# Optimization experiments

Hardware: AMD Instinct MI355X
Metric: run time of the kernel (lower is better)

The kernel has to match this reference:

```python
import jax, jax.numpy as jnp
import numpy as np

B, N, H = 8, 2048, 1024

def setup_inputs() -> dict:
    key = jax.random.key(0)
    ks = jax.random.split(key, 10)
    s = 1.0 / np.sqrt(2 * H)
    return {
        "sem": jax.random.normal(ks[0], (B, N, H), jnp.float32),
        "temp": jax.random.normal(ks[1], (B, N, H), jnp.float32),
        "Wq": jax.random.normal(ks[2], (2 * H, H), jnp.float32) * s,
        "bq": jnp.zeros((H,), jnp.float32),
        "Wk": jax.random.normal(ks[3], (2 * H, H), jnp.float32) * s,
        "bk": jnp.zeros((H,), jnp.float32),
        "Wv": jax.random.normal(ks[4], (2 * H, H), jnp.float32) * s,
        "bv": jnp.zeros((H,), jnp.float32),
        "Wg": jax.random.normal(ks[5], (2 * H, 1), jnp.float32) * s,
        "bg": jnp.zeros((1,), jnp.float32),
    }

def reference(sem, temp, Wq, bq, Wk, bk, Wv, bv, Wg, bg):
    combined = jnp.concatenate([sem, temp], axis=-1)          # [B,N,2H]
    Q = combined @ Wq + bq                                    # [B,N,H]
    K = combined @ Wk + bk
    V = combined @ Wv + bv
    scale = 1.0 / jnp.sqrt(jnp.asarray(Q.shape[-1], Q.dtype))
    scores = jnp.einsum('bqh,bkh->bqk', Q, K) * scale         # [B,N,N]
    attn = jax.nn.softmax(scores, axis=-1)
    gate = jax.nn.sigmoid(combined @ Wg + bg)                 # [B,N,1]
    attn_weights = attn * gate                                # row-wise gate
    fused = jnp.einsum('bqk,bkh->bqh', attn_weights, V)       # [B,N,H]
    return fused + sem, attn_weights.mean(axis=1)             # [B,N,H], [B,N]
```

## Files before the change

kernel.cpp:

```cpp
#include <hip/hip_runtime.h>
#include <stdint.h>
#include <math.h>

#define NB 8
#define NN 2048
#define HH 1024
#define K2 2048
#define MM 16384

typedef unsigned short u16;
typedef __attribute__((ext_vector_type(8))) short short8v;
typedef __attribute__((ext_vector_type(4))) float floatx4;

__device__ __forceinline__ float bf2f(u16 u) { return __uint_as_float(((unsigned)u) << 16); }
__device__ __forceinline__ u16 f2bf(float f) {
  unsigned u = __float_as_uint(f);
  unsigned r = (u + 0x7fffu + ((u >> 16) & 1u)) >> 16;
  return (u16)r;
}

__device__ __forceinline__ void async16(const void* g, void* lds) {
  __builtin_amdgcn_global_load_lds((const __attribute__((address_space(1))) void*)g,
                                   (__attribute__((address_space(3))) void*)lds,
                                   16, 0, 0);
}

__device__ __forceinline__ int xcd_swz(int bid, int nblk) {
  return (bid & 7) * (nblk >> 3) + (bid >> 3);
}

#define SBAR() __builtin_amdgcn_sched_barrier(0)

__device__ __forceinline__ void gemm128_core(const u16* __restrict__ A, int lda,
                                             const u16* __restrict__ Bt, int ldb,
                                             int rowA0, int rowB0, int K,
                                             u16* sA, u16* sB, floatx4 acc[4][4]) {
  const int t = threadIdx.x;
  const int w = t >> 6, l = t & 63;
  const int wr = w >> 1, wc = w & 1;

#pragma unroll
  for (int mi = 0; mi < 4; mi++)
#pragma unroll
    for (int ni = 0; ni < 4; ni++) { floatx4 z = {0.f,0.f,0.f,0.f}; acc[mi][ni] = z; }

  const int srow = l >> 2;
  const int cs = (((l & 3) ^ ((l >> 3) & 3)) << 3);
  const u16* gA0 = A + (size_t)(rowA0 + w * 32 + srow) * lda + cs;
  const u16* gA1 = A + (size_t)(rowA0 + w * 32 + 16 + srow) * lda + cs;
  const u16* gB0 = Bt + (size_t)(rowB0 + w * 32 + srow) * ldb + cs;
  const u16* gB1 = Bt + (size_t)(rowB0 + w * 32 + 16 + srow) * ldb + cs;
  char* dA = (char*)sA + w * 2048 + l * 16;
  char* dB = (char*)sB + w * 2048 + l * 16;

  const int fr = l & 15;
  const int ch = (((l >> 4) ^ ((fr >> 1) & 3)) << 4);
  const int abase = wr * 4096 + fr * 64 + ch;
  const int bbase = wc * 4096 + fr * 64 + ch;

  const int NT = K >> 5;

#define STG128(bi, kt) { const int ko_ = (kt) << 5; const int bo_ = (bi) << 13; \
    async16(gA0 + ko_, dA + bo_); async16(gA1 + ko_, dA + bo_ + 1024);          \
    async16(gB0 + ko_, dB + bo_); async16(gB1 + ko_, dB + bo_ + 1024); }

  STG128(0, 0);
  for (int tt = 0; tt < NT; ++tt) {
    const int bc = tt & 1;
    if (tt + 1 < NT) {
      STG128(bc ^ 1, tt + 1);
      asm volatile("s_waitcnt vmcnt(4)" ::: "memory");
    } else {
      asm volatile("s_waitcnt vmcnt(0)" ::: "memory");
    }
    __builtin_amdgcn_s_barrier();

    const char* a = (const char*)sA + (bc << 13);
    const char* b = (const char*)sB + (bc << 13);
    short8v af[4], bf[4];
#pragma unroll
    for (int mi = 0; mi < 4; mi++) af[mi] = *(const short8v*)(a + abase + mi * 1024);
#pragma unroll
    for (int ni = 0; ni < 4; ni++) bf[ni] = *(const short8v*)(b + bbase + ni * 1024);
    __builtin_amdgcn_s_setprio(1);
#pragma unroll
    for (int mi = 0; mi < 4; mi++)
#pragma unroll
      for (int ni = 0; ni < 4; ni++)
        acc[mi][ni] = __builtin_amdgcn_mfma_f32_16x16x32_bf16(af[mi], bf[ni], acc[mi][ni], 0, 0, 0);
    __builtin_amdgcn_s_setprio(0);
    SBAR();
    __builtin_amdgcn_s_barrier();
  }
#undef STG128
}

__global__ void __launch_bounds__(256) k_prep_gate(const float* __restrict__ sem,
                                                   const float* __restrict__ temp,
                                                   const float* __restrict__ Wg,
                                                   const float* __restrict__ bg,
                                                   u16* __restrict__ X, float* __restrict__ gate) {
  __shared__ float red[4];
  int row = blockIdx.x;
  int t = threadIdx.x, w = t >> 6, l = t & 63;
  const float* s0 = sem + (size_t)row * 1024 + t * 4;
  const float* t0 = temp + (size_t)row * 1024 + t * 4;
  u16* xr = X + (size_t)row * 2048;
  float4 a = *(const float4*)s0;
  float4 b = *(const float4*)t0;
  ushort4 oa = { f2bf(a.x), f2bf(a.y), f2bf(a.z), f2bf(a.w) };
  ushort4 ob = { f2bf(b.x), f2bf(b.y), f2bf(b.z), f2bf(b.w) };
  *(ushort4*)(xr + t * 4) = oa;
  *(ushort4*)(xr + 1024 + t * 4) = ob;
  float4 wa = *(const float4*)(Wg + t * 4);
  float4 wb = *(const float4*)(Wg + 1024 + t * 4);
  float s = a.x * wa.x + a.y * wa.y + a.z * wa.z + a.w * wa.w
          + b.x * wb.x + b.y * wb.y + b.z * wb.z + b.w * wb.w;
#pragma unroll
  for (int off = 32; off > 0; off >>= 1) s += __shfl_xor(s, off);
  if (l == 0) red[w] = s;
  __syncthreads();
  if (t == 0) {
    float tot = red[0] + red[1] + red[2] + red[3] + bg[0];
    gate[row] = 1.f / (1.f + expf(-tot));
  }
}

__global__ void __launch_bounds__(256) k_transpose_w(const float* __restrict__ W,
                                                     u16* __restrict__ Wt) {
  __shared__ float s[32][33];
  int tile = blockIdx.x;
  int nt = tile & 31, kt = tile >> 5;
  int tx = threadIdx.x & 31, ty = threadIdx.x >> 5;
  int n0 = nt << 5, k0 = kt << 5;
#pragma unroll
  for (int j = 0; j < 32; j += 8)
    s[ty + j][tx] = W[(size_t)(k0 + ty + j) * 1024 + (n0 + tx)];
  __syncthreads();
#pragma unroll
  for (int j = 0; j < 32; j += 8)
    Wt[(size_t)(n0 + ty + j) * 2048 + (k0 + tx)] = f2bf(s[tx][ty + j]);
}

__global__ void __launch_bounds__(256, 3) k_proj_qkv(const u16* __restrict__ X,
                                                     const u16* __restrict__ Wt,
                                                     const float* __restrict__ bq,
                                                     const float* __restrict__ bk,
                                                     const float* __restrict__ bv,
                                                     u16* __restrict__ Qb,
                                                     u16* __restrict__ Kb,
                                                     u16* __restrict__ Vt) {
  __shared__ __align__(16) u16 sA[2 * 4096];
  __shared__ __align__(16) u16 sB[2 * 4096];
  int tile = xcd_swz(blockIdx.x, 3072);
  int bm = tile / 24, bn = tile - bm * 24;
  floatx4 acc[4][4];
  gemm128_core(X, K2, Wt, K2, bm * 128, bn * 128, K2, sA, sB, acc);

  const int t = threadIdx.x, w = t >> 6, l = t & 63;
  const int wr = w >> 1, wc = w & 1;
  const int r0 = bm * 128 + wr * 64 + ((l >> 4) << 2);
  const int c0 = (bn & 7) * 128 + wc * 64 + (l & 15);
  const int which = bn >> 3;
  if (which == 2) {
#pragma unroll
    for (int ni = 0; ni < 4; ni++) {
      int h = c0 + ni * 16;
      float bvv = bv[h];
#pragma unroll
      for (int mi = 0; mi < 4; mi++) {
        int rg = r0 + mi * 16;
        int b = rg >> 11, n = rg & 2047;
        ushort4 o = { f2bf(acc[mi][ni][0] + bvv), f2bf(acc[mi][ni][1] + bvv),
                      f2bf(acc[mi][ni][2] + bvv), f2bf(acc[mi][ni][3] + bvv) };
        *(ushort4*)&Vt[((size_t)b * 1024 + h) * 2048 + n] = o;
      }
    }
  } else {
    u16* Out = (which == 0) ? Qb : Kb;
    const float* bias = (which == 0) ? bq : bk;
#pragma unroll
    for (int ni = 0; ni < 4; ni++) {
      int c1 = c0 + ni * 16;
      float bvv = bias[c1];
#pragma unroll
      for (int mi = 0; mi < 4; mi++)
#pragma unroll
        for (int i = 0; i < 4; i++)
          Out[(size_t)(r0 + mi * 16 + i) * 1024 + c1] = f2bf(acc[mi][ni][i] + bvv);
    }
  }
}

__global__ void __launch_bounds__(256, 3) k_scores(const u16* __restrict__ Q, const u16* __restrict__ Kb,
                                                   u16* __restrict__ E, float* __restrict__ lsum) {
  __shared__ __align__(16) u16 sA[2 * 4096];
  __shared__ __align__(16) u16 sB[2 * 4096];
  int tile = xcd_swz(blockIdx.x, 2048);
  int b = tile >> 8, r = tile & 255, bm = r >> 4, bn = r & 15;
  const u16* A = Q + (size_t)b * NN * HH;
  const u16* Bt = Kb + (size_t)b * NN * HH;
  floatx4 acc[4][4];
  gemm128_core(A, HH, Bt, HH, bm * 128, bn * 128, HH, sA, sB, acc);

  u16* Eb = E + (size_t)b * NN * NN;
  float* lb = lsum + b * NN;
  const int t = threadIdx.x, w = t >> 6, l = t & 63;
  const int wr = w >> 1, wc = w & 1;
  const int q0 = bm * 128 + wr * 64 + ((l >> 4) << 2);
  const int k0c = bn * 128 + wc * 64 + (l & 15);
#pragma unroll
  for (int mi = 0; mi < 4; mi++)
#pragma unroll
    for (int i = 0; i < 4; i++) {
      int q = q0 + mi * 16 + i;
      float rs = 0.f;
#pragma unroll
      for (int ni = 0; ni < 4; ni++) {
        float e = expf(acc[mi][ni][i] * 0.03125f);
        Eb[(size_t)q * NN + k0c + ni * 16] = f2bf(e);
        rs += e;
      }
      rs += __shfl_xor(rs, 1);
      rs += __shfl_xor(rs, 2);
      rs += __shfl_xor(rs, 4);
      rs += __shfl_xor(rs, 8);
      if ((l & 15) == 0) atomicAdd(&lb[q], rs);
    }
}

__global__ void __launch_bounds__(256, 3) k_pv(const u16* __restrict__ E, const u16* __restrict__ Vt,
                                               const float* __restrict__ gate, const float* __restrict__ lsum,
                                               const float* __restrict__ sem, float* __restrict__ out) {
  __shared__ __align__(16) u16 sA[2 * 4096];
  __shared__ __align__(16) u16 sB[2 * 4096];
  int tile = xcd_swz(blockIdx.x, 1024);
  int b = tile >> 7, r = tile & 127, bm = r >> 3, bn = r & 7;
  const u16* A = E + (size_t)b * NN * NN;
  const u16* Bt = Vt + (size_t)b * HH * NN;
  floatx4 acc[4][4];
  gemm128_core(A, NN, Bt, NN, bm * 128, bn * 128, NN, sA, sB, acc);

  const int t = threadIdx.x, w = t >> 6, l = t & 63;
  const int wr = w >> 1, wc = w & 1;
  const int q0 = bm * 128 + wr * 64 + ((l >> 4) << 2);
  const int h0 = bn * 128 + wc * 64 + (l & 15);
#pragma unroll
  for (int mi = 0; mi < 4; mi++)
#pragma unroll
    for (int i = 0; i < 4; i++) {
      int q = q0 + mi * 16 + i;
      size_t gq = (size_t)b * NN + q;
      float wq = gate[gq] / lsum[gq];
#pragma unroll
      for (int ni = 0; ni < 4; ni++) {
        int h = h0 + ni * 16;
        out[gq * HH + h] = acc[mi][ni][i] * wq + sem[gq * HH + h];
      }
    }
}

__global__ void __launch_bounds__(256) k_colmean(const u16* __restrict__ E, const float* __restrict__ gate,
                                                 const float* __restrict__ lsum, float* __restrict__ cm) {
  __shared__ float wsh[256];
  int bid = blockIdx.x;
  int b = bid >> 6, rest = bid & 63;
  int ks = rest >> 3, qc = rest & 7;
  int t = threadIdx.x;
  {
    size_t gq = (size_t)b * NN + qc * 256 + t;
    wsh[t] = gate[gq] / lsum[gq];
  }
  __syncthreads();
  int k = ks * 256 + t;
  const u16* Eb = E + ((size_t)b * NN + (size_t)qc * 256) * NN + k;
  float s = 0.f;
  for (int q = 0; q < 256; q++) s += wsh[q] * bf2f(Eb[(size_t)q * NN]);
  atomicAdd(&cm[b * NN + k], s * (1.f / 2048.f));
}

extern "C" void kernel_launch(void* const* d_in, const int* in_sizes, int n_in,
                              void* d_out, int out_size, void* d_ws, size_t ws_size,
                              hipStream_t stream) {
  const float* sem  = (const float*)d_in[0];
  const float* temp = (const float*)d_in[1];
  const float* Wq   = (const float*)d_in[2];
  const float* bq   = (const float*)d_in[3];
  const float* Wk   = (const float*)d_in[4];
  const float* bk   = (const float*)d_in[5];
  const float* Wv   = (const float*)d_in[6];
  const float* bv   = (const float*)d_in[7];
  const float* Wg   = (const float*)d_in[8];
  const float* bg   = (const float*)d_in[9];
  float* out = (float*)d_out;

  char* ws = (char*)d_ws;
  u16* X      = (u16*)ws;
  u16* E      = X;
  u16* WqkvT  = (u16*)(ws + 67108864);
  u16* Qb     = (u16*)(ws + 79691776);
  u16* Kb     = (u16*)(ws + 113246208);
  u16* Vt     = (u16*)(ws + 146800640);
  float* gate = (float*)(ws + 180355072);
  float* lsum = (float*)(ws + 180420608);

  hipMemsetAsync(lsum, 0, 65536, stream);
  hipMemsetAsync(out + 16777216, 0, 65536, stream);

  k_prep_gate<<<16384, 256, 0, stream>>>(sem, temp, Wg, bg, X, gate);
  k_transpose_w<<<2048, 256, 0, stream>>>(Wq, WqkvT);
  k_transpose_w<<<2048, 256, 0, stream>>>(Wk, WqkvT + (size_t)1024 * 2048);
  k_transpose_w<<<2048, 256, 0, stream>>>(Wv, WqkvT + (size_t)2048 * 2048);
  k_proj_qkv<<<3072, 256, 0, stream>>>(X, WqkvT, bq, bk, bv, Qb, Kb, Vt);
  k_scores<<<2048, 256, 0, stream>>>(Qb, Kb, E, lsum);
  k_pv<<<1024, 256, 0, stream>>>(E, Vt, gate, lsum, sem, out);
  k_colmean<<<512, 256, 0, stream>>>(E, gate, lsum, out + 16777216);
}
```

Baseline: 502.2 us.

## Switch GEMM core to 32x32x16 MFMA with triple-buffered LDS pipeline

Replaces the 16x16x32 bf16 MFMA tiles with 32x32x16 MFMAs, each wave holding a 2x2 grid of 32x32 accumulators. LDS fragment reads are restructured to match, and the epilogues of the QKV, scores and PV kernels are remapped to the new accumulator layout. The staging pipeline goes from double to triple buffering, keeping two K-tiles in flight to hide global load latency. The cost is 50% more LDS per block, which may hurt occupancy at 3 blocks per CU. The swizzle and lane mapping must also stay conflict-free and correct.

Measured after the change: 572.7 us. 14.0% more time.

```diff
diff --git a/kernel.cpp b/kernel.cpp
--- a/kernel.cpp
+++ b/kernel.cpp
@@ -10,7 +10,7 @@
 
 typedef unsigned short u16;
 typedef __attribute__((ext_vector_type(8))) short short8v;
-typedef __attribute__((ext_vector_type(4))) float floatx4;
+typedef __attribute__((ext_vector_type(16))) float floatx16;
 
 __device__ __forceinline__ float bf2f(u16 u) { return __uint_as_float(((unsigned)u) << 16); }
 __device__ __forceinline__ u16 f2bf(float f) {
@@ -31,18 +31,20 @@
 
 #define SBAR() __builtin_amdgcn_sched_barrier(0)
 
+#define MFMA32(a, b, c) __builtin_amdgcn_mfma_f32_32x32x16_bf16(a, b, c, 0, 0, 0)
+
 __device__ __forceinline__ void gemm128_core(const u16* __restrict__ A, int lda,
                                              const u16* __restrict__ Bt, int ldb,
                                              int rowA0, int rowB0, int K,
-                                             u16* sA, u16* sB, floatx4 acc[4][4]) {
+                                             u16* sA, u16* sB, floatx16 acc[2][2]) {
   const int t = threadIdx.x;
   const int w = t >> 6, l = t & 63;
   const int wr = w >> 1, wc = w & 1;
 
 #pragma unroll
-  for (int mi = 0; mi < 4; mi++)
-#pragma unroll
-    for (int ni = 0; ni < 4; ni++) { floatx4 z = {0.f,0.f,0.f,0.f}; acc[mi][ni] = z; }
+  for (int mi = 0; mi < 2; mi++)
+#pragma unroll
+    for (int ni = 0; ni < 2; ni++) acc[mi][ni] = (floatx16)(0.f);
 
   const int srow = l >> 2;
   const int cs = (((l & 3) ^ ((l >> 3) & 3)) << 3);
@@ -53,10 +55,10 @@
   char* dA = (char*)sA + w * 2048 + l * 16;
   char* dB = (char*)sB + w * 2048 + l * 16;
 
-  const int fr = l & 15;
-  const int ch = (((l >> 4) ^ ((fr >> 1) & 3)) << 4);
-  const int abase = wr * 4096 + fr * 64 + ch;
-  const int bbase = wc * 4096 + fr * 64 + ch;
+  const int l31 = l & 31;
+  const int arow = (wr * 64 + l31) * 64;
+  const int brow = (wc * 64 + l31) * 64;
+  const int pc0 = (((l >> 5) ^ ((l >> 1) & 3)) << 4);
 
   const int NT = K >> 5;
 
@@ -65,32 +67,43 @@
     async16(gB0 + ko_, dB + bo_); async16(gB1 + ko_, dB + bo_ + 1024); }
 
   STG128(0, 0);
+  STG128(1, 1);
+  int bc = 0, bs = 2;
   for (int tt = 0; tt < NT; ++tt) {
-    const int bc = tt & 1;
-    if (tt + 1 < NT) {
-      STG128(bc ^ 1, tt + 1);
+    if (tt + 2 < NT) {
+      STG128(bs, tt + 2);
+      asm volatile("s_waitcnt vmcnt(8)" ::: "memory");
+    } else if (tt + 1 < NT) {
       asm volatile("s_waitcnt vmcnt(4)" ::: "memory");
     } else {
       asm volatile("s_waitcnt vmcnt(0)" ::: "memory");
     }
     __builtin_amdgcn_s_barrier();
 
-    const char* a = (const char*)sA + (bc << 13);
-    const char* b = (const char*)sB + (bc << 13);
-    short8v af[4], bf[4];
-#pragma unroll
-    for (int mi = 0; mi < 4; mi++) af[mi] = *(const short8v*)(a + abase + mi * 1024);
-#pragma unroll
-    for (int ni = 0; ni < 4; ni++) bf[ni] = *(const short8v*)(b + bbase + ni * 1024);
+    const char* a = (const char*)sA + bc * 8192;
+    const char* b = (const char*)sB + bc * 8192;
+    short8v a00 = *(const short8v*)(a + arow + pc0);
+    short8v a01 = *(const short8v*)(a + arow + (pc0 ^ 32));
+    short8v a10 = *(const short8v*)(a + arow + 2048 + pc0);
+    short8v a11 = *(const short8v*)(a + arow + 2048 + (pc0 ^ 32));
+    short8v b00 = *(const short8v*)(b + brow + pc0);
+    short8v b01 = *(const short8v*)(b + brow + (pc0 ^ 32));
+    short8v b10 = *(const short8v*)(b + brow + 2048 + pc0);
+    short8v b11 = *(const short8v*)(b + brow + 2048 + (pc0 ^ 32));
     __builtin_amdgcn_s_setprio(1);
-#pragma unroll
-    for (int mi = 0; mi < 4; mi++)
-#pragma unroll
-      for (int ni = 0; ni < 4; ni++)
-        acc[mi][ni] = __builtin_amdgcn_mfma_f32_16x16x32_bf16(af[mi], bf[ni], acc[mi][ni], 0, 0, 0);
+    acc[0][0] = MFMA32(a00, b00, acc[0][0]);
+    acc[0][1] = MFMA32(a00, b10, acc[0][1]);
+    acc[1][0] = MFMA32(a10, b00, acc[1][0]);
+    acc[1][1] = MFMA32(a10, b10, acc[1][1]);
+    acc[0][0] = MFMA32(a01, b01, acc[0][0]);
+    acc[0][1] = MFMA32(a01, b11, acc[0][1]);
+    acc[1][0] = MFMA32(a11, b01, acc[1][0]);
+    acc[1][1] = MFMA32(a11, b11, acc[1][1]);
     __builtin_amdgcn_s_setprio(0);
     SBAR();
     __builtin_amdgcn_s_barrier();
+    bc = (bc == 2) ? 0 : bc + 1;
+    bs = (bs == 2) ? 0 : bs + 1;
   }
 #undef STG128
 }
@@ -150,113 +163,117 @@
                                                      u16* __restrict__ Qb,
                                                      u16* __restrict__ Kb,
                                                      u16* __restrict__ Vt) {
-  __shared__ __align__(16) u16 sA[2 * 4096];
-  __shared__ __align__(16) u16 sB[2 * 4096];
+  __shared__ __align__(16) u16 sA[3 * 4096];
+  __shared__ __align__(16) u16 sB[3 * 4096];
   int tile = xcd_swz(blockIdx.x, 3072);
   int bm = tile / 24, bn = tile - bm * 24;
-  floatx4 acc[4][4];
+  floatx16 acc[2][2];
   gemm128_core(X, K2, Wt, K2, bm * 128, bn * 128, K2, sA, sB, acc);
 
   const int t = threadIdx.x, w = t >> 6, l = t & 63;
   const int wr = w >> 1, wc = w & 1;
-  const int r0 = bm * 128 + wr * 64 + ((l >> 4) << 2);
-  const int c0 = (bn & 7) * 128 + wc * 64 + (l & 15);
+  const int l31 = l & 31, lh = l >> 5;
+  const int r0 = bm * 128 + wr * 64;
+  const int c0b = (bn & 7) * 128 + wc * 64;
   const int which = bn >> 3;
   if (which == 2) {
 #pragma unroll
-    for (int ni = 0; ni < 4; ni++) {
-      int h = c0 + ni * 16;
-      float bvv = bv[h];
-#pragma unroll
-      for (int mi = 0; mi < 4; mi++) {
-        int rg = r0 + mi * 16;
-        int b = rg >> 11, n = rg & 2047;
-        ushort4 o = { f2bf(acc[mi][ni][0] + bvv), f2bf(acc[mi][ni][1] + bvv),
-                      f2bf(acc[mi][ni][2] + bvv), f2bf(acc[mi][ni][3] + bvv) };
-        *(ushort4*)&Vt[((size_t)b * 1024 + h) * 2048 + n] = o;
+    for (int mi = 0; mi < 2; mi++)
+#pragma unroll
+      for (int ni = 0; ni < 2; ni++) {
+        int h = c0b + ni * 32 + l31;
+        float bvv = bv[h];
+#pragma unroll
+        for (int g = 0; g < 4; g++) {
+          int rg = r0 + mi * 32 + 8 * g + 4 * lh;
+          int b = rg >> 11, n = rg & 2047;
+          ushort4 o = { f2bf(acc[mi][ni][4 * g + 0] + bvv), f2bf(acc[mi][ni][4 * g + 1] + bvv),
+                        f2bf(acc[mi][ni][4 * g + 2] + bvv), f2bf(acc[mi][ni][4 * g + 3] + bvv) };
+          *(ushort4*)&Vt[((size_t)b * 1024 + h) * 2048 + n] = o;
+        }
       }
-    }
   } else {
     u16* Out = (which == 0) ? Qb : Kb;
     const float* bias = (which == 0) ? bq : bk;
 #pragma unroll
-    for (int ni = 0; ni < 4; ni++) {
-      int c1 = c0 + ni * 16;
-      float bvv = bias[c1];
-#pragma unroll
-      for (int mi = 0; mi < 4; mi++)
-#pragma unroll
-        for (int i = 0; i < 4; i++)
-          Out[(size_t)(r0 + mi * 16 + i) * 1024 + c1] = f2bf(acc[mi][ni][i] + bvv);
-    }
+    for (int mi = 0; mi < 2; mi++)
+#pragma unroll
+      for (int ni = 0; ni < 2; ni++) {
+        int c1 = c0b + ni * 32 + l31;
+        float bvv = bias[c1];
+#pragma unroll
+        for (int r = 0; r < 16; r++) {
+          int row = r0 + mi * 32 + (r & 3) + 8 * (r >> 2) + 4 * lh;
+          Out[(size_t)row * 1024 + c1] = f2bf(acc[mi][ni][r] + bvv);
+        }
+      }
   }
 }
 
 __global__ void __launch_bounds__(256, 3) k_scores(const u16* __restrict__ Q, const u16* __restrict__ Kb,
                                                    u16* __restrict__ E, float* __restrict__ lsum) {
-  __shared__ __align__(16) u16 sA[2 * 4096];
-  __shared__ __align__(16) u16 sB[2 * 4096];
+  __shared__ __align__(16) u16 sA[3 * 4096];
+  __shared__ __align__(16) u16 sB[3 * 4096];
   int tile = xcd_swz(blockIdx.x, 2048);
   int b = tile >> 8, r = tile & 255, bm = r >> 4, bn = r & 15;
   const u16* A = Q + (size_t)b * NN * HH;
   const u16* Bt = Kb + (size_t)b * NN * HH;
-  floatx4 acc[4][4];
+  floatx16 acc[2][2];
   gemm128_core(A, HH, Bt, HH, bm * 128, bn * 128, HH, sA, sB, acc);
 
   u16* Eb = E + (size_t)b * NN * NN;
   float* lb = lsum + b * NN;
   const int t = threadIdx.x, w = t >> 6, l = t & 63;
   const int wr = w >> 1, wc = w & 1;
-  const int q0 = bm * 128 + wr * 64 + ((l >> 4) << 2);
-  const int k0c = bn * 128 + wc * 64 + (l & 15);
-#pragma unroll
-  for (int mi = 0; mi < 4; mi++)
-#pragma unroll
-    for (int i = 0; i < 4; i++) {
-      int q = q0 + mi * 16 + i;
-      float rs = 0.f;
-#pragma unroll
-      for (int ni = 0; ni < 4; ni++) {
-        float e = expf(acc[mi][ni][i] * 0.03125f);
-        Eb[(size_t)q * NN + k0c + ni * 16] = f2bf(e);
-        rs += e;
-      }
+  const int l31 = l & 31, lh = l >> 5;
+  const int q0 = bm * 128 + wr * 64;
+  const int k0c = bn * 128 + wc * 64;
+#pragma unroll
+  for (int mi = 0; mi < 2; mi++)
+#pragma unroll
+    for (int r = 0; r < 16; r++) {
+      int q = q0 + mi * 32 + (r & 3) + 8 * (r >> 2) + 4 * lh;
+      float e0 = expf(acc[mi][0][r] * 0.03125f);
+      float e1 = expf(acc[mi][1][r] * 0.03125f);
+      Eb[(size_t)q * NN + k0c + l31] = f2bf(e0);
+      Eb[(size_t)q * NN + k0c + 32 + l31] = f2bf(e1);
+      float rs = e0 + e1;
       rs += __shfl_xor(rs, 1);
       rs += __shfl_xor(rs, 2);
       rs += __shfl_xor(rs, 4);
       rs += __shfl_xor(rs, 8);
-      if ((l & 15) == 0) atomicAdd(&lb[q], rs);
+      rs += __shfl_xor(rs, 16);
+      if (l31 == 0) atomicAdd(&lb[q], rs);
     }
 }
 
 __global__ void __launch_bounds__(256, 3) k_pv(const u16* __restrict__ E, const u16* __restrict__ Vt,
                                                const float* __restrict__ gate, const float* __restrict__ lsum,
                                                const float* __restrict__ sem, float* __restrict__ out) {
-  __shared__ __align__(16) u16 sA[2 * 4096];
-  __shared__ __align__(16) u16 sB[2 * 4096];
+  __shared__ __align__(16) u16 sA[3 * 4096];
+  __shared__ __align__(16) u16 sB[3 * 4096];
   int tile = xcd_swz(blockIdx.x, 1024);
   int b = tile >> 7, r = tile & 127, bm = r >> 3, bn = r & 7;
   const u16* A = E + (size_t)b * NN * NN;
   const u16* Bt = Vt + (size_t)b * HH * NN;
-  floatx4 acc[4][4];
+  floatx16 acc[2][2];
   gemm128_core(A, NN, Bt, NN, bm * 128, bn * 128, NN, sA, sB, acc);
 
   const int t = threadIdx.x, w = t >> 6, l = t & 63;
   const int wr = w >> 1, wc = w & 1;
-  const int q0 = bm * 128 + wr * 64 + ((l >> 4) << 2);
-  const int h0 = bn * 128 + wc * 64 + (l & 15);
-#pragma unroll
-  for (int mi = 0; mi < 4; mi++)
-#pragma unroll
-    for (int i = 0; i < 4; i++) {
-      int q = q0 + mi * 16 + i;
+  const int l31 = l & 31, lh = l >> 5;
+  const int q0 = bm * 128 + wr * 64;
+  const int h0 = bn * 128 + wc * 64;
+#pragma unroll
+  for (int mi = 0; mi < 2; mi++)
+#pragma unroll
+    for (int r = 0; r < 16; r++) {
+      int q = q0 + mi * 32 + (r & 3) + 8 * (r >> 2) + 4 * lh;
       size_t gq = (size_t)b * NN + q;
       float wq = gate[gq] / lsum[gq];
-#pragma unroll
-      for (int ni = 0; ni < 4; ni++) {
-        int h = h0 + ni * 16;
-        out[gq * HH + h] = acc[mi][ni][i] * wq + sem[gq * HH + h];
-      }
+      int h = h0 + l31;
+      out[gq * HH + h] = acc[mi][0][r] * wq + sem[gq * HH + h];
+      out[gq * HH + h + 32] = acc[mi][1][r] * wq + sem[gq * HH + h + 32];
     }
 }
 
```
